# Optimization experiments

Measured on AMD Instinct MI355X. Metric: run time of the kernel, lower is better.

The kernel has to match this reference:

```python
import jax, jax.numpy as jnp
import numpy as np

N, E, G = 25600, 409600, 128   # nodes, edges, graphs
IN, H, C = 200, 4, 64          # raw feat dim, heads, hidden_channels
IN2 = 2 * IN                   # after NaN-mask concat
BN_EPS = 1e-5

def _glorot(key, shape):
    lim = float(np.sqrt(6.0 / (shape[0] + shape[-1])))
    return jax.random.uniform(key, shape, jnp.float32, -lim, lim)

def setup_inputs():
    key = jax.random.key(0)
    k = iter(jax.random.split(key, 40))
    inp = {
        "x": jax.random.normal(next(k), (N, IN), jnp.float32),
        "edge_index": jax.random.randint(next(k), (2, E), 0, N, jnp.int32),
        "edge_attr": jax.random.normal(next(k), (E, 1), jnp.float32),
        "batch": jnp.repeat(jnp.arange(G, dtype=jnp.int32), N // G),
    }
    dims = [(IN2, H, C), (H * C, H, C), (H * C, 1, C)]
    for i, (din, h, c) in enumerate(dims):
        inp[f"W{i}"] = _glorot(next(k), (din, h * c))
        inp[f"as{i}"] = _glorot(next(k), (h, c))
        inp[f"ad{i}"] = _glorot(next(k), (h, c))
        inp[f"We{i}"] = _glorot(next(k), (1, h * c))
        inp[f"ae{i}"] = _glorot(next(k), (h, c))
        inp[f"b{i}"] = jnp.zeros((h * c,), jnp.float32)
    inp["bn_g"] = jnp.ones((H * C,), jnp.float32)
    inp["bn_b"] = jnp.zeros((H * C,), jnp.float32)
    inp["bn_m"] = jnp.zeros((H * C,), jnp.float32)
    inp["bn_v"] = jnp.ones((H * C,), jnp.float32)
    inp["cw1"] = _glorot(next(k), (C, C))
    inp["cb1"] = jnp.zeros((C,), jnp.float32)
    inp["cw2"] = _glorot(next(k), (C, 2))
    inp["cb2"] = jnp.zeros((2,), jnp.float32)
    return inp

def _gat(x, src, dst, ea, W, att_s, att_d, We, att_e, b, heads, ch):
    """PyG GATConv (edge_dim=1, add_self_loops=True, fill_value='mean', concat=True)."""
    n = x.shape[0]
    # self-loop edge_attr = mean of incoming edge_attr per destination node
    cnt = jax.ops.segment_sum(jnp.ones((ea.shape[0], 1), ea.dtype), dst, n)
    loop_ea = jax.ops.segment_sum(ea, dst, n) / jnp.maximum(cnt, 1.0)
    idx = jnp.arange(n, dtype=src.dtype)
    src = jnp.concatenate([src, idx])
    dst = jnp.concatenate([dst, idx])
    ea = jnp.concatenate([ea, loop_ea], axis=0)
    h = (x @ W).reshape(n, heads, ch)                      # [N,H,C]
    a_s = jnp.einsum('nhc,hc->nh', h, att_s)
    a_d = jnp.einsum('nhc,hc->nh', h, att_d)
    a_e = jnp.einsum('ehc,hc->eh', (ea @ We).reshape(-1, heads, ch), att_e)
    alpha = jax.nn.leaky_relu(a_s[src] + a_d[dst] + a_e, 0.2)   # [E',H]
    # segment softmax over destination neighborhoods
    m = jax.ops.segment_max(alpha, dst, n)
    ex = jnp.exp(alpha - m[dst])
    z = jax.ops.segment_sum(ex, dst, n)
    alpha = ex / (z[dst] + 1e-16)
    out = jax.ops.segment_sum(h[src] * alpha[:, :, None], dst, n)  # [N,H,C]
    return out.reshape(n, heads * ch) + b

def reference(x, edge_index, edge_attr, batch,
              W0, as0, ad0, We0, ae0, b0,
              W1, as1, ad1, We1, ae1, b1,
              W2, as2, ad2, We2, ae2, b2,
              bn_g, bn_b, bn_m, bn_v, cw1, cb1, cw2, cb2):
    nan_mask = jnp.isnan(x).astype(x.dtype)
    x = jnp.concatenate([jnp.nan_to_num(x), nan_mask], axis=-1)   # [N, 2*IN]
    edge_attr = jnp.nan_to_num(edge_attr)
    src, dst = edge_index[0], edge_index[1]
    for (W, a_s, a_d, We, a_e, b) in [(W0, as0, ad0, We0, ae0, b0),
                                      (W1, as1, ad1, We1, ae1, b1)]:
        x = _gat(x, src, dst, edge_attr, W, a_s, a_d, We, a_e, b, H, C)
        x = (x - bn_m) / jnp.sqrt(bn_v + BN_EPS) * bn_g + bn_b    # eval-mode BN
        x = jax.nn.relu(x)                                        # dropout = identity (eval)
    x = _gat(x, src, dst, edge_attr, W2, as2, ad2, We2, ae2, b2, 1, C)
    # global mean pool over graphs
    cnt = jax.ops.segment_sum(jnp.ones((x.shape[0], 1), x.dtype), batch, G)
    g = jax.ops.segment_sum(x, batch, G) / jnp.maximum(cnt, 1.0)  # [G, C]
    hdn = jax.nn.gelu(g @ cw1 + cb1, approximate=False)
    return hdn @ cw2 + cb2                                        # [G, 2]
```

## Files before the change

### kernel.cpp

```cpp
#include <hip/hip_runtime.h>
#include <hip/hip_bf16.h>

static const int kN  = 25600;
static const int kE  = 409600;
static const int kG  = 128;
static const int kNPG = 200;
static const int kIN = 200;
static const int kIN2 = 400;
#define BN_EPS_ 1e-5f

typedef __attribute__((ext_vector_type(8))) short short8;
typedef __attribute__((ext_vector_type(4))) float f32x4;

__device__ __forceinline__ float bu(ushort u) {
  union { float f; unsigned u32; } x; x.u32 = ((unsigned)u) << 16; return x.f;
}
__device__ __forceinline__ ushort f2u(float v) {
  __hip_bfloat16 t = __float2bfloat16(v);
  return *(ushort*)&t;
}

__device__ __forceinline__ float wredSum(float v) {
#pragma unroll
  for (int off = 1; off < 64; off <<= 1) v += __shfl_xor(v, off, 64);
  return v;
}

__device__ __forceinline__ float lrelu(float a) { return (a > 0.f) ? a : 0.2f * a; }

__global__ void k_zero(unsigned int* __restrict__ p, int n) {
  int i = blockIdx.x * blockDim.x + threadIdx.x;
  if (i < n) p[i] = 0u;
}


__global__ void k_prep_x(const float* __restrict__ x, ushort* __restrict__ x2) {
  int i = blockIdx.x * blockDim.x + threadIdx.x;
  if (i >= kN * kIN) return;
  int n = i / kIN, j = i - n * kIN;
  float v = x[i];
  bool bad = (v != v);
  x2[(size_t)n * kIN2 + j] = f2u(bad ? 0.f : v);
  x2[(size_t)n * kIN2 + kIN + j] = f2u(bad ? 1.f : 0.f);
}

__global__ void k_prep_wt(const float* __restrict__ W, ushort* __restrict__ Wt,
                          int K, int N) {
  int i = blockIdx.x * blockDim.x + threadIdx.x;
  if (i >= K * N) return;
  int n = i / K, k = i - n * K;
  Wt[(size_t)n * K + k] = f2u(W[(size_t)k * N + n]);
}

__global__ void k_wedot_all(const float* __restrict__ We0, const float* __restrict__ ae0,
                            const float* __restrict__ We1, const float* __restrict__ ae1,
                            const float* __restrict__ We2, const float* __restrict__ ae2,
                            float* __restrict__ wed) {
  int b = blockIdx.x, tid = threadIdx.x;
  const float* We = (b == 0) ? We0 : (b == 1) ? We1 : We2;
  const float* ae = (b == 0) ? ae0 : (b == 1) ? ae1 : ae2;
  int n = (b == 2) ? 64 : 256;
  float v = (tid < n) ? We[tid] * ae[tid] : 0.f;
  v = wredSum(v);
  if ((tid & 63) == 0 && tid < n) wed[b * 4 + (tid >> 6)] = v;
}

__global__ void k_edge_cnt(const int* __restrict__ ei, int* __restrict__ deg,
                           int* __restrict__ epos) {
  int e = blockIdx.x * blockDim.x + threadIdx.x;
  if (e >= kE) return;
  epos[e] = atomicAdd(&deg[ei[kE + e]], 1);
}

__global__ void k_scan_chunk(const int* __restrict__ deg, int* __restrict__ rowp,
                             int* __restrict__ csum) {
  __shared__ int s[1024];
  int tid = threadIdx.x;
  int i = blockIdx.x * 1024 + tid;
  int v = deg[i];
  s[tid] = v;
  __syncthreads();
  for (int off = 1; off < 1024; off <<= 1) {
    int t = (tid >= off) ? s[tid - off] : 0;
    __syncthreads();
    s[tid] += t;
    __syncthreads();
  }
  rowp[i] = s[tid] - v;
  if (tid == 1023) csum[blockIdx.x] = s[tid];
}

__global__ void k_scan_sums(const int* __restrict__ csum, int* __restrict__ coff, int nchunk) {
  if (threadIdx.x == 0 && blockIdx.x == 0) {
    int acc = 0;
    for (int i = 0; i < nchunk; i++) { coff[i] = acc; acc += csum[i]; }
  }
}

__global__ void k_scan_fix(int* __restrict__ rowp, const int* __restrict__ coff) {
  int i = blockIdx.x * blockDim.x + threadIdx.x;
  if (i >= kN) return;
  rowp[i] += coff[i >> 10];
}

__global__ void k_scatter_n(const int* __restrict__ ei, const float* __restrict__ ea,
                            const int* __restrict__ rowp, const int* __restrict__ epos,
                            int* __restrict__ esrc, float* __restrict__ eaC) {
  int e = blockIdx.x * blockDim.x + threadIdx.x;
  if (e >= kE) return;
  int d = ei[kE + e];
  int slot = rowp[d] + d + epos[e];
  esrc[slot] = ei[e];
  float v = ea[e];
  if (v != v) v = 0.f;
  eaC[slot] = v;
}

__global__ void k_selfloop(const int* __restrict__ rowp, const int* __restrict__ deg,
                           int* __restrict__ esrc, float* __restrict__ eaC) {
  int n = blockIdx.x * 4 + (threadIdx.x >> 6);
  int lane = threadIdx.x & 63;
  int start = rowp[n] + n;
  int dg = deg[n];
  float s = 0.f;
  for (int k = lane; k < dg; k += 64) s += eaC[start + k];
  s = wredSum(s);
  if (lane == 0) {
    esrc[start + dg] = n;
    eaC[start + dg] = s / fmaxf((float)dg, 1.f);
  }
}

#define GBK 64
#define GPAD 72

template <int BN>
__global__ __launch_bounds__(256) void k_gemm_f(const ushort* __restrict__ A,
                                                const ushort* __restrict__ Bt,
                                                ushort* __restrict__ C,
                                                const float* __restrict__ as_g,
                                                const float* __restrict__ ad_g,
                                                float* __restrict__ a_sg,
                                                float* __restrict__ a_dg, int K) {
  constexpr int MI = (BN == 256) ? 4 : 1;
  constexpr int H = (BN == 256) ? 4 : 1;
  __shared__ ushort As[64 * GPAD];
  __shared__ ushort Bs[BN * GPAD];
  int tid = threadIdx.x;
  int lane = tid & 63, w = tid >> 6;
  int l15 = lane & 15, l4 = lane >> 4;
  int row0 = blockIdx.y * 64;
  int wr = (BN == 256) ? 0 : (w * 16);
  int wc = (BN == 256) ? (w * 64) : 0;
  f32x4 acc[MI][4] = {};

  int ach = tid & 7;
  int arow = tid >> 3;

  for (int kt = 0; kt < K; kt += GBK) {
    __syncthreads();
#pragma unroll
    for (int p = 0; p < 2; p++) {
      int r = p * 32 + arow;
      int kg = kt + ach * 8;
      short8 v = {0, 0, 0, 0, 0, 0, 0, 0};
      if (kg < K) v = *(const short8*)&A[(size_t)(row0 + r) * K + kg];
      *(short8*)&As[r * GPAD + ach * 8] = v;
    }
#pragma unroll
    for (int p = 0; p < BN / 32; p++) {
      int r = p * 32 + arow;
      int kg = kt + ach * 8;
      short8 v = {0, 0, 0, 0, 0, 0, 0, 0};
      if (kg < K) v = *(const short8*)&Bt[(size_t)r * K + kg];
      *(short8*)&Bs[r * GPAD + ach * 8] = v;
    }
    __syncthreads();
#pragma unroll
    for (int kk = 0; kk < 2; kk++) {
      short8 af[MI], bf[4];
#pragma unroll
      for (int mi = 0; mi < MI; mi++)
        af[mi] = *(const short8*)&As[(wr + mi * 16 + l15) * GPAD + kk * 32 + l4 * 8];
#pragma unroll
      for (int ni = 0; ni < 4; ni++)
        bf[ni] = *(const short8*)&Bs[(wc + ni * 16 + l15) * GPAD + kk * 32 + l4 * 8];
#pragma unroll
      for (int mi = 0; mi < MI; mi++)
#pragma unroll
        for (int ni = 0; ni < 4; ni++)
          acc[mi][ni] = __builtin_amdgcn_mfma_f32_16x16x32_bf16(af[mi], bf[ni],
                                                                acc[mi][ni], 0, 0, 0);
    }
  }
#pragma unroll
  for (int mi = 0; mi < MI; mi++) {
    int rbase = row0 + wr + mi * 16 + l4 * 4;
#pragma unroll
    for (int ni = 0; ni < 4; ni++) {
      int col = wc + ni * 16 + l15;
#pragma unroll
      for (int r = 0; r < 4; r++)
        C[(size_t)(rbase + r) * BN + col] = f2u(acc[mi][ni][r]);
    }
  }
  float asv[4], adv[4];
#pragma unroll
  for (int ni = 0; ni < 4; ni++) {
    asv[ni] = as_g[wc + ni * 16 + l15];
    adv[ni] = ad_g[wc + ni * 16 + l15];
  }
  int hh = (BN == 256) ? w : 0;
#pragma unroll
  for (int mi = 0; mi < MI; mi++) {
#pragma unroll
    for (int r = 0; r < 4; r++) {
      float ps = 0.f, pd = 0.f;
#pragma unroll
      for (int ni = 0; ni < 4; ni++) {
        ps += acc[mi][ni][r] * asv[ni];
        pd += acc[mi][ni][r] * adv[ni];
      }
#pragma unroll
      for (int off = 1; off < 16; off <<= 1) {
        ps += __shfl_xor(ps, off, 64);
        pd += __shfl_xor(pd, off, 64);
      }
      if (l15 == 0) {
        int row = row0 + wr + mi * 16 + l4 * 4 + r;
        a_sg[row * H + hh] = ps;
        a_dg[row * H + hh] = pd;
      }
    }
  }
}

__global__ __launch_bounds__(256) void k_agg4(
    const ushort* __restrict__ hbuf, const int* __restrict__ rowp,
    const int* __restrict__ deg, const int* __restrict__ esrc,
    const float* __restrict__ eaC, const float* __restrict__ a_s,
    const float* __restrict__ a_d, const float* __restrict__ wed,
    const float* __restrict__ bias, const float* __restrict__ bng,
    const float* __restrict__ bnb, const float* __restrict__ bnm,
    const float* __restrict__ bnv, ushort* __restrict__ xout) {
  int tid = threadIdx.x;
  int w = tid >> 6, lane = tid & 63;
  int d = blockIdx.x * 4 + w;
  int start = rowp[d] + d;
  int total = deg[d] + 1;
  int h = lane >> 4;
  float adh = a_d[d * 4 + h];
  float wdh = wed[h];

  int c0 = lane * 4;
  float a0 = 0.f, a1 = 0.f, a2 = 0.f, a3 = 0.f, sz = 0.f;
  int k = 0;
  for (; k + 4 <= total; k += 4) {
    int s0 = esrc[start + k], s1 = esrc[start + k + 1];
    int s2 = esrc[start + k + 2], s3 = esrc[start + k + 3];
    float e0 = eaC[start + k], e1 = eaC[start + k + 1];
    float e2 = eaC[start + k + 2], e3 = eaC[start + k + 3];
    ushort4 v0 = *(const ushort4*)&hbuf[(size_t)s0 * 256 + c0];
    ushort4 v1 = *(const ushort4*)&hbuf[(size_t)s1 * 256 + c0];
    ushort4 v2 = *(const ushort4*)&hbuf[(size_t)s2 * 256 + c0];
    ushort4 v3 = *(const ushort4*)&hbuf[(size_t)s3 * 256 + c0];
    float w0 = __expf(lrelu(a_s[s0 * 4 + h] + adh + e0 * wdh));
    float w1 = __expf(lrelu(a_s[s1 * 4 + h] + adh + e1 * wdh));
    float w2 = __expf(lrelu(a_s[s2 * 4 + h] + adh + e2 * wdh));
    float w3 = __expf(lrelu(a_s[s3 * 4 + h] + adh + e3 * wdh));
    sz += (w0 + w1) + (w2 + w3);
    a0 += w0 * bu(v0.x) + w1 * bu(v1.x) + w2 * bu(v2.x) + w3 * bu(v3.x);
    a1 += w0 * bu(v0.y) + w1 * bu(v1.y) + w2 * bu(v2.y) + w3 * bu(v3.y);
    a2 += w0 * bu(v0.z) + w1 * bu(v1.z) + w2 * bu(v2.z) + w3 * bu(v3.z);
    a3 += w0 * bu(v0.w) + w1 * bu(v1.w) + w2 * bu(v2.w) + w3 * bu(v3.w);
  }
  for (; k < total; k++) {
    int s0 = esrc[start + k];
    float e0 = eaC[start + k];
    ushort4 v0 = *(const ushort4*)&hbuf[(size_t)s0 * 256 + c0];
    float w0 = __expf(lrelu(a_s[s0 * 4 + h] + adh + e0 * wdh));
    sz += w0;
    a0 += w0 * bu(v0.x); a1 += w0 * bu(v0.y);
    a2 += w0 * bu(v0.z); a3 += w0 * bu(v0.w);
  }
  float winv = 1.f / (sz + 1e-16f);
  a0 *= winv; a1 *= winv; a2 *= winv; a3 *= winv;

  float4 bi = *(const float4*)&bias[c0];
  a0 += bi.x; a1 += bi.y; a2 += bi.z; a3 += bi.w;
  float4 g4 = *(const float4*)&bng[c0], b4 = *(const float4*)&bnb[c0];
  float4 m4 = *(const float4*)&bnm[c0], v4 = *(const float4*)&bnv[c0];
  a0 = fmaxf((a0 - m4.x) * rsqrtf(v4.x + BN_EPS_) * g4.x + b4.x, 0.f);
  a1 = fmaxf((a1 - m4.y) * rsqrtf(v4.y + BN_EPS_) * g4.y + b4.y, 0.f);
  a2 = fmaxf((a2 - m4.z) * rsqrtf(v4.z + BN_EPS_) * g4.z + b4.z, 0.f);
  a3 = fmaxf((a3 - m4.w) * rsqrtf(v4.w + BN_EPS_) * g4.w + b4.w, 0.f);
  ushort4 o = make_ushort4(f2u(a0), f2u(a1), f2u(a2), f2u(a3));
  *(ushort4*)&xout[(size_t)d * 256 + c0] = o;
}

__global__ __launch_bounds__(256) void k_agg1(
    const ushort* __restrict__ hbuf, const int* __restrict__ rowp,
    const int* __restrict__ deg, const int* __restrict__ esrc,
    const float* __restrict__ eaC, const float* __restrict__ a_s,
    const float* __restrict__ a_d, const float* __restrict__ wed,
    const float* __restrict__ bias, float* __restrict__ xout) {
  int tid = threadIdx.x;
  int w = tid >> 6, lane = tid & 63;
  int d = blockIdx.x * 4 + w;
  int start = rowp[d] + d;
  int total = deg[d] + 1;
  float adh = a_d[d];
  float wdh = wed[0];

  float acc = 0.f, sz = 0.f;
  int k = 0;
  for (; k + 4 <= total; k += 4) {
    int s0 = esrc[start + k], s1 = esrc[start + k + 1];
    int s2 = esrc[start + k + 2], s3 = esrc[start + k + 3];
    float e0 = eaC[start + k], e1 = eaC[start + k + 1];
    float e2 = eaC[start + k + 2], e3 = eaC[start + k + 3];
    float v0 = bu(hbuf[(size_t)s0 * 64 + lane]);
    float v1 = bu(hbuf[(size_t)s1 * 64 + lane]);
    float v2 = bu(hbuf[(size_t)s2 * 64 + lane]);
    float v3 = bu(hbuf[(size_t)s3 * 64 + lane]);
    float w0 = __expf(lrelu(a_s[s0] + adh + e0 * wdh));
    float w1 = __expf(lrelu(a_s[s1] + adh + e1 * wdh));
    float w2 = __expf(lrelu(a_s[s2] + adh + e2 * wdh));
    float w3 = __expf(lrelu(a_s[s3] + adh + e3 * wdh));
    sz += (w0 + w1) + (w2 + w3);
    acc += w0 * v0 + w1 * v1 + w2 * v2 + w3 * v3;
  }
  for (; k < total; k++) {
    int s0 = esrc[start + k];
    float w0 = __expf(lrelu(a_s[s0] + adh + eaC[start + k] * wdh));
    sz += w0;
    acc += w0 * bu(hbuf[(size_t)s0 * 64 + lane]);
  }
  acc = acc / (sz + 1e-16f) + bias[lane];
  xout[(size_t)d * 64 + lane] = acc;
}

__global__ void k_poolhead(const float* __restrict__ xin,
                           const float* __restrict__ cw1, const float* __restrict__ cb1,
                           const float* __restrict__ cw2, const float* __restrict__ cb2,
                           float* __restrict__ out) {
  __shared__ float part[4][64];
  __shared__ float gb[64], hb[64];
  int g = blockIdx.x, tid = threadIdx.x;
  int c = tid & 63, w = tid >> 6;
  float acc = 0.f;
  size_t base = (size_t)g * kNPG * 64;
  for (int n = w; n < kNPG; n += 4) acc += xin[base + (size_t)n * 64 + c];
  part[w][c] = acc;
  __syncthreads();
  if (tid < 64) {
    float s = (part[0][c] + part[1][c]) + (part[2][c] + part[3][c]);
    gb[c] = s * (1.f / kNPG);
  }
  __syncthreads();
  if (tid < 64) {
    float s = cb1[c];
#pragma unroll 8
    for (int i = 0; i < 64; i++) s += gb[i] * cw1[i * 64 + c];
    s = 0.5f * s * (1.f + erff(s * 0.70710678118654752f));
    hb[c] = s;
  }
  __syncthreads();
  if (tid < 2) {
    float o = cb2[tid];
    for (int i = 0; i < 64; i++) o += hb[i] * cw2[i * 2 + tid];
    out[g * 2 + tid] = o;
  }
}


extern "C" void kernel_launch(void* const* d_in, const int* in_sizes, int n_in,
                              void* d_out, int out_size, void* d_ws, size_t ws_size,
                              hipStream_t stream) {
  (void)in_sizes; (void)n_in; (void)out_size; (void)ws_size;
  const float* x  = (const float*)d_in[0];
  const int* ei   = (const int*)d_in[1];
  const float* ea = (const float*)d_in[2];
  const float *W[3], *as_[3], *ad_[3], *We[3], *ae[3], *bi[3];
  for (int l = 0; l < 3; l++) {
    W[l]   = (const float*)d_in[4 + l * 6 + 0];
    as_[l] = (const float*)d_in[4 + l * 6 + 1];
    ad_[l] = (const float*)d_in[4 + l * 6 + 2];
    We[l]  = (const float*)d_in[4 + l * 6 + 3];
    ae[l]  = (const float*)d_in[4 + l * 6 + 4];
    bi[l]  = (const float*)d_in[4 + l * 6 + 5];
  }
  const float* bng = (const float*)d_in[22];
  const float* bnb = (const float*)d_in[23];
  const float* bnm = (const float*)d_in[24];
  const float* bnv = (const float*)d_in[25];
  const float* cw1 = (const float*)d_in[26];
  const float* cb1 = (const float*)d_in[27];
  const float* cw2 = (const float*)d_in[28];
  const float* cb2 = (const float*)d_in[29];

  char* p = (char*)d_ws;
  auto alloc = [&](size_t bytes) -> void* {
    void* r = (void*)p;
    p += (bytes + 255) & ~(size_t)255;
    return r;
  };
  ushort* x2b   = (ushort*)alloc((size_t)kN * kIN2 * 2);
  ushort* hbufb = (ushort*)alloc((size_t)kN * 256 * 2);
  ushort* xbA   = (ushort*)alloc((size_t)kN * 256 * 2);
  ushort* xbB   = (ushort*)alloc((size_t)kN * 256 * 2);
  float*  fbuf  = (float*)alloc((size_t)kN * 64 * 4);
  ushort* Wt0   = (ushort*)alloc((size_t)kIN2 * 256 * 2);
  ushort* Wt1   = (ushort*)alloc((size_t)256 * 256 * 2);
  ushort* Wt2   = (ushort*)alloc((size_t)256 * 64 * 2);
  float* a_s    = (float*)alloc((size_t)kN * 4 * 4);
  float* a_d    = (float*)alloc((size_t)kN * 4 * 4);
  int* rowp     = (int*)alloc((size_t)kN * 4);
  int* esrc     = (int*)alloc((size_t)(kE + kN) * 4);
  float* eaC    = (float*)alloc((size_t)(kE + kN) * 4);
  int* epos     = (int*)alloc((size_t)kE * 4);
  float* wed    = (float*)alloc(256);
  int* csum     = (int*)alloc(256);
  int* coff     = (int*)alloc(256);
  int* deg      = (int*)alloc((size_t)kN * 4);
  k_zero<<<(kN + 255) / 256, 256, 0, stream>>>((unsigned int*)deg, kN);

  k_prep_x<<<(kN * kIN + 255) / 256, 256, 0, stream>>>(x, x2b);
  k_prep_wt<<<(kIN2 * 256 + 255) / 256, 256, 0, stream>>>(W[0], Wt0, kIN2, 256);
  k_prep_wt<<<(256 * 256 + 255) / 256, 256, 0, stream>>>(W[1], Wt1, 256, 256);
  k_prep_wt<<<(256 * 64 + 255) / 256, 256, 0, stream>>>(W[2], Wt2, 256, 64);
  k_wedot_all<<<3, 256, 0, stream>>>(We[0], ae[0], We[1], ae[1], We[2], ae[2], wed);
  k_edge_cnt<<<(kE + 255) / 256, 256, 0, stream>>>(ei, deg, epos);
  k_scan_chunk<<<kN / 1024, 1024, 0, stream>>>(deg, rowp, csum);
  k_scan_sums<<<1, 64, 0, stream>>>(csum, coff, kN / 1024);
  k_scan_fix<<<(kN + 255) / 256, 256, 0, stream>>>(rowp, coff);
  k_scatter_n<<<(kE + 255) / 256, 256, 0, stream>>>(ei, ea, rowp, epos, esrc, eaC);
  k_selfloop<<<kN / 4, 256, 0, stream>>>(rowp, deg, esrc, eaC);

  int Kd[3] = {kIN2, 256, 256};
  const ushort* Ain[3] = {x2b, xbA, xbB};
  const ushort* Wt[3] = {Wt0, Wt1, Wt2};
  ushort* loutB[2] = {xbA, xbB};
  dim3 gg(1, kN / 64);

  for (int l = 0; l < 3; l++) {
    if (l < 2)
      k_gemm_f<256><<<gg, 256, 0, stream>>>(Ain[l], Wt[l], hbufb, as_[l], ad_[l],
                                            a_s, a_d, Kd[l]);
    else
      k_gemm_f<64><<<gg, 256, 0, stream>>>(Ain[l], Wt[l], hbufb, as_[l], ad_[l],
                                           a_s, a_d, Kd[l]);
    if (l < 2)
      k_agg4<<<kN / 4, 256, 0, stream>>>(hbufb, rowp, deg, esrc, eaC, a_s, a_d,
                                         &wed[l * 4], bi[l], bng, bnb, bnm, bnv,
                                         loutB[l]);
    else
      k_agg1<<<kN / 4, 256, 0, stream>>>(hbufb, rowp, deg, esrc, eaC, a_s, a_d,
                                         &wed[8], bi[l], fbuf);
  }

  k_poolhead<<<kG, 256, 0, stream>>>(fbuf, cw1, cb1, cw2, cb2, (float*)d_out);
}
```

Before: 344.6 us.

## Fuse GAT aggregation with next-layer GEMM and merge prep/scan kernels

Merges zeroing, input prep, weight transposes and edge-weight dots into one launch, and replaces the three-kernel scan with a single-block scan. Fuses layer-0 aggregation plus BN/ReLU into the layer-1 GEMM and layer-1 aggregation into the layer-2 GEMM through shared memory, so the intermediate activations are never written to or re-read from global memory. The first GEMM moves to 32-row tiles. The aim is to cut launch overhead and global traffic, at the cost of fewer parallel blocks and aggregation work serialized within each block ahead of the MFMA phase.

```diff
diff --git a/kernel.cpp b/kernel.cpp
--- a/kernel.cpp
+++ b/kernel.cpp
@@ -19,50 +19,60 @@
   __hip_bfloat16 t = __float2bfloat16(v);
   return *(ushort*)&t;
 }
-
 __device__ __forceinline__ float wredSum(float v) {
 #pragma unroll
   for (int off = 1; off < 64; off <<= 1) v += __shfl_xor(v, off, 64);
   return v;
 }
-
 __device__ __forceinline__ float lrelu(float a) { return (a > 0.f) ? a : 0.2f * a; }
 
-__global__ void k_zero(unsigned int* __restrict__ p, int n) {
-  int i = blockIdx.x * blockDim.x + threadIdx.x;
-  if (i < n) p[i] = 0u;
-}
-
-
-__global__ void k_prep_x(const float* __restrict__ x, ushort* __restrict__ x2) {
-  int i = blockIdx.x * blockDim.x + threadIdx.x;
-  if (i >= kN * kIN) return;
-  int n = i / kIN, j = i - n * kIN;
-  float v = x[i];
-  bool bad = (v != v);
-  x2[(size_t)n * kIN2 + j] = f2u(bad ? 0.f : v);
-  x2[(size_t)n * kIN2 + kIN + j] = f2u(bad ? 1.f : 0.f);
-}
-
-__global__ void k_prep_wt(const float* __restrict__ W, ushort* __restrict__ Wt,
-                          int K, int N) {
-  int i = blockIdx.x * blockDim.x + threadIdx.x;
-  if (i >= K * N) return;
-  int n = i / K, k = i - n * K;
-  Wt[(size_t)n * K + k] = f2u(W[(size_t)k * N + n]);
-}
-
-__global__ void k_wedot_all(const float* __restrict__ We0, const float* __restrict__ ae0,
-                            const float* __restrict__ We1, const float* __restrict__ ae1,
-                            const float* __restrict__ We2, const float* __restrict__ ae2,
-                            float* __restrict__ wed) {
+__global__ void k_pre(const float* __restrict__ x, ushort* __restrict__ x2,
+                      int* __restrict__ deg,
+                      const float* __restrict__ W0, ushort* __restrict__ Wt0,
+                      const float* __restrict__ W1, ushort* __restrict__ Wt1,
+                      const float* __restrict__ W2, ushort* __restrict__ Wt2,
+                      const float* __restrict__ We0, const float* __restrict__ ae0,
+                      const float* __restrict__ We1, const float* __restrict__ ae1,
+                      const float* __restrict__ We2, const float* __restrict__ ae2,
+                      float* __restrict__ wed) {
   int b = blockIdx.x, tid = threadIdx.x;
-  const float* We = (b == 0) ? We0 : (b == 1) ? We1 : We2;
-  const float* ae = (b == 0) ? ae0 : (b == 1) ? ae1 : ae2;
-  int n = (b == 2) ? 64 : 256;
-  float v = (tid < n) ? We[tid] * ae[tid] : 0.f;
-  v = wredSum(v);
-  if ((tid & 63) == 0 && tid < n) wed[b * 4 + (tid >> 6)] = v;
+  if (b < 100) {
+    deg[b * 256 + tid] = 0;
+    return;
+  }
+  if (b < 20100) {
+    int i = (b - 100) * 256 + tid;
+    int n = i / kIN, j = i - n * kIN;
+    float v = x[i];
+    bool bad = (v != v);
+    x2[(size_t)n * kIN2 + j] = f2u(bad ? 0.f : v);
+    x2[(size_t)n * kIN2 + kIN + j] = f2u(bad ? 1.f : 0.f);
+    return;
+  }
+  int pb = b - 20100;
+  if (pb >= 720) {
+    int l = pb - 720;
+    const float* We = (l == 0) ? We0 : (l == 1) ? We1 : We2;
+    const float* ae = (l == 0) ? ae0 : (l == 1) ? ae1 : ae2;
+    int n = (l == 2) ? 64 : 256;
+    float v = (tid < n) ? We[tid] * ae[tid] : 0.f;
+    v = wredSum(v);
+    if ((tid & 63) == 0 && tid < n) wed[l * 4 + (tid >> 6)] = v;
+    return;
+  }
+  int i = pb * 256 + tid;
+  if (i < 102400) {
+    int n = i / kIN2, k = i - n * kIN2;
+    Wt0[(size_t)n * kIN2 + k] = f2u(W0[(size_t)k * 256 + n]);
+  } else if (i < 102400 + 65536) {
+    int j = i - 102400;
+    int n = j >> 8, k = j & 255;
+    Wt1[(size_t)n * 256 + k] = f2u(W1[(size_t)k * 256 + n]);
+  } else {
+    int j = i - 102400 - 65536;
+    int n = j >> 8, k = j & 255;
+    Wt2[(size_t)n * 256 + k] = f2u(W2[(size_t)k * 64 + n]);
+  }
 }
 
 __global__ void k_edge_cnt(const int* __restrict__ ei, int* __restrict__ deg,
@@ -72,35 +82,25 @@
   epos[e] = atomicAdd(&deg[ei[kE + e]], 1);
 }
 
-__global__ void k_scan_chunk(const int* __restrict__ deg, int* __restrict__ rowp,
-                             int* __restrict__ csum) {
+__global__ void k_scan_all(const int* __restrict__ deg, int* __restrict__ rowp) {
   __shared__ int s[1024];
-  int tid = threadIdx.x;
-  int i = blockIdx.x * 1024 + tid;
-  int v = deg[i];
-  s[tid] = v;
+  int t = threadIdx.x;
+  int base = t * 25;
+  int loc[25];
+  int sum = 0;
+#pragma unroll
+  for (int i = 0; i < 25; i++) { loc[i] = sum; sum += deg[base + i]; }
+  s[t] = sum;
   __syncthreads();
   for (int off = 1; off < 1024; off <<= 1) {
-    int t = (tid >= off) ? s[tid - off] : 0;
+    int v = (t >= off) ? s[t - off] : 0;
     __syncthreads();
-    s[tid] += t;
+    s[t] += v;
     __syncthreads();
   }
-  rowp[i] = s[tid] - v;
-  if (tid == 1023) csum[blockIdx.x] = s[tid];
-}
-
-__global__ void k_scan_sums(const int* __restrict__ csum, int* __restrict__ coff, int nchunk) {
-  if (threadIdx.x == 0 && blockIdx.x == 0) {
-    int acc = 0;
-    for (int i = 0; i < nchunk; i++) { coff[i] = acc; acc += csum[i]; }
-  }
-}
-
-__global__ void k_scan_fix(int* __restrict__ rowp, const int* __restrict__ coff) {
-  int i = blockIdx.x * blockDim.x + threadIdx.x;
-  if (i >= kN) return;
-  rowp[i] += coff[i >> 10];
+  int excl = s[t] - sum;
+#pragma unroll
+  for (int i = 0; i < 25; i++) rowp[base + i] = excl + loc[i];
 }
 
 __global__ void k_scatter_n(const int* __restrict__ ei, const float* __restrict__ ea,
@@ -133,42 +133,35 @@
 
 #define GBK 64
 #define GPAD 72
-
-template <int BN>
-__global__ __launch_bounds__(256) void k_gemm_f(const ushort* __restrict__ A,
-                                                const ushort* __restrict__ Bt,
-                                                ushort* __restrict__ C,
-                                                const float* __restrict__ as_g,
-                                                const float* __restrict__ ad_g,
-                                                float* __restrict__ a_sg,
-                                                float* __restrict__ a_dg, int K) {
-  constexpr int MI = (BN == 256) ? 4 : 1;
-  constexpr int H = (BN == 256) ? 4 : 1;
-  __shared__ ushort As[64 * GPAD];
-  __shared__ ushort Bs[BN * GPAD];
+#define APAD 264
+
+__global__ __launch_bounds__(256) void k_gemm0(const ushort* __restrict__ A,
+                                               const ushort* __restrict__ Bt,
+                                               ushort* __restrict__ C,
+                                               const float* __restrict__ as_g,
+                                               const float* __restrict__ ad_g,
+                                               float* __restrict__ a_sg,
+                                               float* __restrict__ a_dg, int K) {
+  __shared__ ushort As[32 * GPAD];
+  __shared__ ushort Bs[256 * GPAD];
   int tid = threadIdx.x;
   int lane = tid & 63, w = tid >> 6;
   int l15 = lane & 15, l4 = lane >> 4;
-  int row0 = blockIdx.y * 64;
-  int wr = (BN == 256) ? 0 : (w * 16);
-  int wc = (BN == 256) ? (w * 64) : 0;
-  f32x4 acc[MI][4] = {};
-
-  int ach = tid & 7;
-  int arow = tid >> 3;
+  int row0 = blockIdx.y * 32;
+  f32x4 acc[2][4] = {};
+  int ach = tid & 7, arow = tid >> 3;
 
   for (int kt = 0; kt < K; kt += GBK) {
     __syncthreads();
-#pragma unroll
-    for (int p = 0; p < 2; p++) {
-      int r = p * 32 + arow;
+    {
+      int r = arow;
       int kg = kt + ach * 8;
       short8 v = {0, 0, 0, 0, 0, 0, 0, 0};
       if (kg < K) v = *(const short8*)&A[(size_t)(row0 + r) * K + kg];
       *(short8*)&As[r * GPAD + ach * 8] = v;
     }
 #pragma unroll
-    for (int p = 0; p < BN / 32; p++) {
+    for (int p = 0; p < 8; p++) {
       int r = p * 32 + arow;
       int kg = kt + ach * 8;
       short8 v = {0, 0, 0, 0, 0, 0, 0, 0};
@@ -178,15 +171,15 @@
     __syncthreads();
 #pragma unroll
     for (int kk = 0; kk < 2; kk++) {
-      short8 af[MI], bf[4];
-#pragma unroll
-      for (int mi = 0; mi < MI; mi++)
-        af[mi] = *(const short8*)&As[(wr + mi * 16 + l15) * GPAD + kk * 32 + l4 * 8];
+      short8 af[2], bf[4];
+#pragma unroll
+      for (int mi = 0; mi < 2; mi++)
+        af[mi] = *(const short8*)&As[(mi * 16 + l15) * GPAD + kk * 32 + l4 * 8];
 #pragma unroll
       for (int ni = 0; ni < 4; ni++)
-        bf[ni] = *(const short8*)&Bs[(wc + ni * 16 + l15) * GPAD + kk * 32 + l4 * 8];
-#pragma unroll
-      for (int mi = 0; mi < MI; mi++)
+        bf[ni] = *(const short8*)&Bs[(w * 64 + ni * 16 + l15) * GPAD + kk * 32 + l4 * 8];
+#pragma unroll
+      for (int mi = 0; mi < 2; mi++)
 #pragma unroll
         for (int ni = 0; ni < 4; ni++)
           acc[mi][ni] = __builtin_amdgcn_mfma_f32_16x16x32_bf16(af[mi], bf[ni],
@@ -194,25 +187,24 @@
     }
   }
 #pragma unroll
-  for (int mi = 0; mi < MI; mi++) {
-    int rbase = row0 + wr + mi * 16 + l4 * 4;
+  for (int mi = 0; mi < 2; mi++) {
+    int rbase = row0 + mi * 16 + l4 * 4;
 #pragma unroll
     for (int ni = 0; ni < 4; ni++) {
-      int col = wc + ni * 16 + l15;
+      int col = w * 64 + ni * 16 + l15;
 #pragma unroll
       for (int r = 0; r < 4; r++)
-        C[(size_t)(rbase + r) * BN + col] = f2u(acc[mi][ni][r]);
+        C[(size_t)(rbase + r) * 256 + col] = f2u(acc[mi][ni][r]);
     }
   }
   float asv[4], adv[4];
 #pragma unroll
   for (int ni = 0; ni < 4; ni++) {
-    asv[ni] = as_g[wc + ni * 16 + l15];
-    adv[ni] = ad_g[wc + ni * 16 + l15];
-  }
-  int hh = (BN == 256) ? w : 0;
-#pragma unroll
-  for (int mi = 0; mi < MI; mi++) {
+    asv[ni] = as_g[w * 64 + ni * 16 + l15];
+    adv[ni] = ad_g[w * 64 + ni * 16 + l15];
+  }
+#pragma unroll
+  for (int mi = 0; mi < 2; mi++) {
 #pragma unroll
     for (int r = 0; r < 4; r++) {
       float ps = 0.f, pd = 0.f;
@@ -227,32 +219,19 @@
         pd += __shfl_xor(pd, off, 64);
       }
       if (l15 == 0) {
-        int row = row0 + wr + mi * 16 + l4 * 4 + r;
-        a_sg[row * H + hh] = ps;
-        a_dg[row * H + hh] = pd;
+        int row = row0 + mi * 16 + l4 * 4 + r;
+        a_sg[row * 4 + w] = ps;
+        a_dg[row * 4 + w] = pd;
       }
     }
   }
 }
 
-__global__ __launch_bounds__(256) void k_agg4(
-    const ushort* __restrict__ hbuf, const int* __restrict__ rowp,
-    const int* __restrict__ deg, const int* __restrict__ esrc,
+__device__ __forceinline__ ushort4 agg_node(
+    const ushort* __restrict__ hbuf, const int* __restrict__ esrc,
     const float* __restrict__ eaC, const float* __restrict__ a_s,
-    const float* __restrict__ a_d, const float* __restrict__ wed,
-    const float* __restrict__ bias, const float* __restrict__ bng,
-    const float* __restrict__ bnb, const float* __restrict__ bnm,
-    const float* __restrict__ bnv, ushort* __restrict__ xout) {
-  int tid = threadIdx.x;
-  int w = tid >> 6, lane = tid & 63;
-  int d = blockIdx.x * 4 + w;
-  int start = rowp[d] + d;
-  int total = deg[d] + 1;
-  int h = lane >> 4;
-  float adh = a_d[d * 4 + h];
-  float wdh = wed[h];
-
-  int c0 = lane * 4;
+    float adh, float wdh, int start, int total, int c0, int h,
+    float4 bi, float4 g4, float4 b4, float4 m4, float4 v4) {
   float a0 = 0.f, a1 = 0.f, a2 = 0.f, a3 = 0.f, sz = 0.f;
   int k = 0;
   for (; k + 4 <= total; k += 4) {
@@ -284,18 +263,193 @@
     a2 += w0 * bu(v0.z); a3 += w0 * bu(v0.w);
   }
   float winv = 1.f / (sz + 1e-16f);
-  a0 *= winv; a1 *= winv; a2 *= winv; a3 *= winv;
-
-  float4 bi = *(const float4*)&bias[c0];
-  a0 += bi.x; a1 += bi.y; a2 += bi.z; a3 += bi.w;
-  float4 g4 = *(const float4*)&bng[c0], b4 = *(const float4*)&bnb[c0];
-  float4 m4 = *(const float4*)&bnm[c0], v4 = *(const float4*)&bnv[c0];
+  a0 = a0 * winv + bi.x; a1 = a1 * winv + bi.y;
+  a2 = a2 * winv + bi.z; a3 = a3 * winv + bi.w;
   a0 = fmaxf((a0 - m4.x) * rsqrtf(v4.x + BN_EPS_) * g4.x + b4.x, 0.f);
   a1 = fmaxf((a1 - m4.y) * rsqrtf(v4.y + BN_EPS_) * g4.y + b4.y, 0.f);
   a2 = fmaxf((a2 - m4.z) * rsqrtf(v4.z + BN_EPS_) * g4.z + b4.z, 0.f);
   a3 = fmaxf((a3 - m4.w) * rsqrtf(v4.w + BN_EPS_) * g4.w + b4.w, 0.f);
-  ushort4 o = make_ushort4(f2u(a0), f2u(a1), f2u(a2), f2u(a3));
-  *(ushort4*)&xout[(size_t)d * 256 + c0] = o;
+  return make_ushort4(f2u(a0), f2u(a1), f2u(a2), f2u(a3));
+}
+
+__global__ __launch_bounds__(256) void k_fuse1(
+    const ushort* __restrict__ hb_in, const int* __restrict__ rowp,
+    const int* __restrict__ deg, const int* __restrict__ esrc,
+    const float* __restrict__ eaC, const float* __restrict__ a_s0,
+    const float* __restrict__ a_d0, const float* __restrict__ wed0,
+    const float* __restrict__ bi0, const float* __restrict__ bng,
+    const float* __restrict__ bnb, const float* __restrict__ bnm,
+    const float* __restrict__ bnv, const ushort* __restrict__ Bt,
+    ushort* __restrict__ C, const float* __restrict__ as1,
+    const float* __restrict__ ad1, float* __restrict__ a_s1,
+    float* __restrict__ a_d1) {
+  __shared__ ushort As[32 * APAD];
+  __shared__ ushort Bs[256 * GPAD];
+  int tid = threadIdx.x;
+  int lane = tid & 63, w = tid >> 6;
+  int l15 = lane & 15, l4 = lane >> 4;
+  int r0 = blockIdx.x * 32;
+  int c0 = lane * 4, h = lane >> 4;
+  float wdh = wed0[h];
+  float4 bi = *(const float4*)&bi0[c0];
+  float4 g4 = *(const float4*)&bng[c0], b4 = *(const float4*)&bnb[c0];
+  float4 m4 = *(const float4*)&bnm[c0], v4 = *(const float4*)&bnv[c0];
+
+  for (int i = 0; i < 8; i++) {
+    int d = r0 + w * 8 + i;
+    int start = rowp[d] + d, total = deg[d] + 1;
+    float adh = a_d0[d * 4 + h];
+    ushort4 o = agg_node(hb_in, esrc, eaC, a_s0, adh, wdh, start, total,
+                         c0, h, bi, g4, b4, m4, v4);
+    *(ushort4*)&As[(w * 8 + i) * APAD + c0] = o;
+  }
+  f32x4 acc[2][4] = {};
+  int ach = tid & 7, arow = tid >> 3;
+  for (int kt = 0; kt < 256; kt += GBK) {
+    __syncthreads();
+#pragma unroll
+    for (int p = 0; p < 8; p++) {
+      int r = p * 32 + arow;
+      *(short8*)&Bs[r * GPAD + ach * 8] =
+          *(const short8*)&Bt[(size_t)r * 256 + kt + ach * 8];
+    }
+    __syncthreads();
+#pragma unroll
+    for (int kk = 0; kk < 2; kk++) {
+      short8 af[2], bf[4];
+#pragma unroll
+      for (int mi = 0; mi < 2; mi++)
+        af[mi] = *(const short8*)&As[(mi * 16 + l15) * APAD + kt + kk * 32 + l4 * 8];
+#pragma unroll
+      for (int ni = 0; ni < 4; ni++)
+        bf[ni] = *(const short8*)&Bs[(w * 64 + ni * 16 + l15) * GPAD + kk * 32 + l4 * 8];
+#pragma unroll
+      for (int mi = 0; mi < 2; mi++)
+#pragma unroll
+        for (int ni = 0; ni < 4; ni++)
+          acc[mi][ni] = __builtin_amdgcn_mfma_f32_16x16x32_bf16(af[mi], bf[ni],
+                                                                acc[mi][ni], 0, 0, 0);
+    }
+  }
+#pragma unroll
+  for (int mi = 0; mi < 2; mi++) {
+    int rbase = r0 + mi * 16 + l4 * 4;
+#pragma unroll
+    for (int ni = 0; ni < 4; ni++) {
+      int col = w * 64 + ni * 16 + l15;
+#pragma unroll
+      for (int r = 0; r < 4; r++)
+        C[(size_t)(rbase + r) * 256 + col] = f2u(acc[mi][ni][r]);
+    }
+  }
+  float asv[4], adv[4];
+#pragma unroll
+  for (int ni = 0; ni < 4; ni++) {
+    asv[ni] = as1[w * 64 + ni * 16 + l15];
+    adv[ni] = ad1[w * 64 + ni * 16 + l15];
+  }
+#pragma unroll
+  for (int mi = 0; mi < 2; mi++) {
+#pragma unroll
+    for (int r = 0; r < 4; r++) {
+      float ps = 0.f, pd = 0.f;
+#pragma unroll
+      for (int ni = 0; ni < 4; ni++) {
+        ps += acc[mi][ni][r] * asv[ni];
+        pd += acc[mi][ni][r] * adv[ni];
+      }
+#pragma unroll
+      for (int off = 1; off < 16; off <<= 1) {
+        ps += __shfl_xor(ps, off, 64);
+        pd += __shfl_xor(pd, off, 64);
+      }
+      if (l15 == 0) {
+        int row = r0 + mi * 16 + l4 * 4 + r;
+        a_s1[row * 4 + w] = ps;
+        a_d1[row * 4 + w] = pd;
+      }
+    }
+  }
+}
+
+__global__ __launch_bounds__(256) void k_fuse2(
+    const ushort* __restrict__ hb_in, const int* __restrict__ rowp,
+    const int* __restrict__ deg, const int* __restrict__ esrc,
+    const float* __restrict__ eaC, const float* __restrict__ a_s1,
+    const float* __restrict__ a_d1, const float* __restrict__ wed1,
+    const float* __restrict__ bi1, const float* __restrict__ bng,
+    const float* __restrict__ bnb, const float* __restrict__ bnm,
+    const float* __restrict__ bnv, const ushort* __restrict__ Bt,
+    ushort* __restrict__ C, const float* __restrict__ as2,
+    const float* __restrict__ ad2, float* __restrict__ a_s2,
+    float* __restrict__ a_d2) {
+  __shared__ ushort As[64 * APAD];
+  __shared__ ushort Bs[64 * APAD];
+  int tid = threadIdx.x;
+  int lane = tid & 63, w = tid >> 6;
+  int l15 = lane & 15, l4 = lane >> 4;
+  int r0 = blockIdx.x * 64;
+  int c0 = lane * 4, h = lane >> 4;
+  for (int idx = tid; idx < 64 * 32; idx += 256) {
+    int r = idx >> 5, ch = idx & 31;
+    *(short8*)&Bs[r * APAD + ch * 8] = *(const short8*)&Bt[(size_t)r * 256 + ch * 8];
+  }
+  float wdh = wed1[h];
+  float4 bi = *(const float4*)&bi1[c0];
+  float4 g4 = *(const float4*)&bng[c0], b4 = *(const float4*)&bnb[c0];
+  float4 m4 = *(const float4*)&bnm[c0], v4 = *(const float4*)&bnv[c0];
+  for (int i = 0; i < 16; i++) {
+    int d = r0 + w * 16 + i;
+    int start = rowp[d] + d, total = deg[d] + 1;
+    float adh = a_d1[d * 4 + h];
+    ushort4 o = agg_node(hb_in, esrc, eaC, a_s1, adh, wdh, start, total,
+                         c0, h, bi, g4, b4, m4, v4);
+    *(ushort4*)&As[(w * 16 + i) * APAD + c0] = o;
+  }
+  __syncthreads();
+  f32x4 acc[4] = {};
+#pragma unroll
+  for (int kk = 0; kk < 8; kk++) {
+    short8 af = *(const short8*)&As[(w * 16 + l15) * APAD + kk * 32 + l4 * 8];
+#pragma unroll
+    for (int ni = 0; ni < 4; ni++) {
+      short8 bf = *(const short8*)&Bs[(ni * 16 + l15) * APAD + kk * 32 + l4 * 8];
+      acc[ni] = __builtin_amdgcn_mfma_f32_16x16x32_bf16(af, bf, acc[ni], 0, 0, 0);
+    }
+  }
+  int rbase = r0 + w * 16 + l4 * 4;
+#pragma unroll
+  for (int ni = 0; ni < 4; ni++) {
+    int col = ni * 16 + l15;
+#pragma unroll
+    for (int r = 0; r < 4; r++)
+      C[(size_t)(rbase + r) * 64 + col] = f2u(acc[ni][r]);
+  }
+  float asv[4], adv[4];
+#pragma unroll
+  for (int ni = 0; ni < 4; ni++) {
+    asv[ni] = as2[ni * 16 + l15];
+    adv[ni] = ad2[ni * 16 + l15];
+  }
+#pragma unroll
+  for (int r = 0; r < 4; r++) {
+    float ps = 0.f, pd = 0.f;
+#pragma unroll
+    for (int ni = 0; ni < 4; ni++) {
+      ps += acc[ni][r] * asv[ni];
+      pd += acc[ni][r] * adv[ni];
+    }
+#pragma unroll
+    for (int off = 1; off < 16; off <<= 1) {
+      ps += __shfl_xor(ps, off, 64);
+      pd += __shfl_xor(pd, off, 64);
+    }
+    if (l15 == 0) {
+      int row = rbase + r;
+      a_s2[row] = ps;
+      a_d2[row] = pd;
+    }
+  }
 }
 
 __global__ __launch_bounds__(256) void k_agg1(
@@ -406,58 +560,42 @@
     return r;
   };
   ushort* x2b   = (ushort*)alloc((size_t)kN * kIN2 * 2);
-  ushort* hbufb = (ushort*)alloc((size_t)kN * 256 * 2);
-  ushort* xbA   = (ushort*)alloc((size_t)kN * 256 * 2);
-  ushort* xbB   = (ushort*)alloc((size_t)kN * 256 * 2);
+  ushort* hbuf0 = (ushort*)alloc((size_t)kN * 256 * 2);
+  ushort* hbuf1 = (ushort*)alloc((size_t)kN * 256 * 2);
+  ushort* h2    = (ushort*)alloc((size_t)kN * 64 * 2);
   float*  fbuf  = (float*)alloc((size_t)kN * 64 * 4);
   ushort* Wt0   = (ushort*)alloc((size_t)kIN2 * 256 * 2);
   ushort* Wt1   = (ushort*)alloc((size_t)256 * 256 * 2);
   ushort* Wt2   = (ushort*)alloc((size_t)256 * 64 * 2);
-  float* a_s    = (float*)alloc((size_t)kN * 4 * 4);
-  float* a_d    = (float*)alloc((size_t)kN * 4 * 4);
+  float* a_s0   = (float*)alloc((size_t)kN * 4 * 4);
+  float* a_d0   = (float*)alloc((size_t)kN * 4 * 4);
+  float* a_s1   = (float*)alloc((size_t)kN * 4 * 4);
+  float* a_d1   = (float*)alloc((size_t)kN * 4 * 4);
+  float* a_s2   = (float*)alloc((size_t)kN * 4);
+  float* a_d2   = (float*)alloc((size_t)kN * 4);
   int* rowp     = (int*)alloc((size_t)kN * 4);
   int* esrc     = (int*)alloc((size_t)(kE + kN) * 4);
   float* eaC    = (float*)alloc((size_t)(kE + kN) * 4);
   int* epos     = (int*)alloc((size_t)kE * 4);
   float* wed    = (float*)alloc(256);
-  int* csum     = (int*)alloc(256);
-  int* coff     = (int*)alloc(256);
   int* deg      = (int*)alloc((size_t)kN * 4);
-  k_zero<<<(kN + 255) / 256, 256, 0, stream>>>((unsigned int*)deg, kN);
-
-  k_prep_x<<<(kN * kIN + 255) / 256, 256, 0, stream>>>(x, x2b);
-  k_prep_wt<<<(kIN2 * 256 + 255) / 256, 256, 0, stream>>>(W[0], Wt0, kIN2, 256);
-  k_prep_wt<<<(256 * 256 + 255) / 256, 256, 0, stream>>>(W[1], Wt1, 256, 256);
-  k_prep_wt<<<(256 * 64 + 255) / 256, 256, 0, stream>>>(W[2], Wt2, 256, 64);
-  k_wedot_all<<<3, 256, 0, stream>>>(We[0], ae[0], We[1], ae[1], We[2], ae[2], wed);
+
+  k_pre<<<100 + 20000 + 723, 256, 0, stream>>>(x, x2b, deg, W[0], Wt0, W[1], Wt1,
+                                               W[2], Wt2, We[0], ae[0], We[1], ae[1],
+                                               We[2], ae[2], wed);
   k_edge_cnt<<<(kE + 255) / 256, 256, 0, stream>>>(ei, deg, epos);
-  k_scan_chunk<<<kN / 1024, 1024, 0, stream>>>(deg, rowp, csum);
-  k_scan_sums<<<1, 64, 0, stream>>>(csum, coff, kN / 1024);
-  k_scan_fix<<<(kN + 255) / 256, 256, 0, stream>>>(rowp, coff);
+  k_scan_all<<<1, 1024, 0, stream>>>(deg, rowp);
   k_scatter_n<<<(kE + 255) / 256, 256, 0, stream>>>(ei, ea, rowp, epos, esrc, eaC);
   k_selfloop<<<kN / 4, 256, 0, stream>>>(rowp, deg, esrc, eaC);
-
-  int Kd[3] = {kIN2, 256, 256};
-  const ushort* Ain[3] = {x2b, xbA, xbB};
-  const ushort* Wt[3] = {Wt0, Wt1, Wt2};
-  ushort* loutB[2] = {xbA, xbB};
-  dim3 gg(1, kN / 64);
-
-  for (int l = 0; l < 3; l++) {
-    if (l < 2)
-      k_gemm_f<256><<<gg, 256, 0, stream>>>(Ain[l], Wt[l], hbufb, as_[l], ad_[l],
-                                            a_s, a_d, Kd[l]);
-    else
-      k_gemm_f<64><<<gg, 256, 0, stream>>>(Ain[l], Wt[l], hbufb, as_[l], ad_[l],
-                                           a_s, a_d, Kd[l]);
-    if (l < 2)
-      k_agg4<<<kN / 4, 256, 0, stream>>>(hbufb, rowp, deg, esrc, eaC, a_s, a_d,
-                                         &wed[l * 4], bi[l], bng, bnb, bnm, bnv,
-                                         loutB[l]);
-    else
-      k_agg1<<<kN / 4, 256, 0, stream>>>(hbufb, rowp, deg, esrc, eaC, a_s, a_d,
-                                         &wed[8], bi[l], fbuf);
-  }
-
+  dim3 gg0(1, kN / 32);
+  k_gemm0<<<gg0, 256, 0, stream>>>(x2b, Wt0, hbuf0, as_[0], ad_[0], a_s0, a_d0, kIN2);
+  k_fuse1<<<kN / 32, 256, 0, stream>>>(hbuf0, rowp, deg, esrc, eaC, a_s0, a_d0,
+                                       &wed[0], bi[0], bng, bnb, bnm, bnv, Wt1,
+                                       hbuf1, as_[1], ad_[1], a_s1, a_d1);
+  k_fuse2<<<kN / 64, 256, 0, stream>>>(hbuf1, rowp, deg, esrc, eaC, a_s1, a_d1,
+                                       &wed[4], bi[1], bng, bnb, bnm, bnv, Wt2,
+                                       h2, as_[2], ad_[2], a_s2, a_d2);
+  k_agg1<<<kN / 4, 256, 0, stream>>>(h2, rowp, deg, esrc, eaC, a_s2, a_d2,
+                                     &wed[8], bi[2], fbuf);
   k_poolhead<<<kG, 256, 0, stream>>>(fbuf, cw1, cb1, cw2, cb2, (float*)d_out);
 }
```

Result: slower. 415.7 us (+20.6%).
